# Performance work log

Hardware: AMD Instinct MI355X
Metric: run time of the kernel (lower is better)

## Reference

```python
import jax, jax.numpy as jnp
import numpy as np

H = 32          # hidden_size
L = 10          # linear_size
EPS = 1e-14


def _lstm_cell(x, h, c, Wih, Whh, bih, bhh):
    # torch LSTMCell: gates ordered [i, f, g, o]
    gates = x @ Wih.T + bih + h @ Whh.T + bhh
    i, f, g, o = jnp.split(gates, 4, axis=-1)
    i = jax.nn.sigmoid(i)
    f = jax.nn.sigmoid(f)
    g = jnp.tanh(g)
    o = jax.nn.sigmoid(o)
    c_new = f * c + i * g
    h_new = o * jnp.tanh(c_new)
    return h_new, c_new


def setup_inputs() -> dict:
    key = jax.random.key(0)
    ks = jax.random.split(key, 24)
    B, N = 8, 100000
    inp = {
        "x": jax.random.normal(ks[0], (B, N), jnp.float32),
        "grad": jax.random.normal(ks[1], (B, N), jnp.float32),
        "h0": jax.random.normal(ks[2], (B, N, H), jnp.float32),
        "c0": jax.random.normal(ks[3], (B, N, H), jnp.float32),
        "h1": jax.random.normal(ks[4], (B, N, H), jnp.float32),
        "c1": jax.random.normal(ks[5], (B, N, H), jnp.float32),
        # initial_transform: Linear(2, L) -> tanh -> Linear(L, L)
        "W1": jax.random.normal(ks[6], (L, 2), jnp.float32) * 0.3,
        "b1": jax.random.normal(ks[7], (L,), jnp.float32) * 0.1,
        "W2": jax.random.normal(ks[8], (L, L), jnp.float32) * 0.3,
        "b2": jax.random.normal(ks[9], (L,), jnp.float32) * 0.1,
        # LSTMCell layer 0 (input L) and layer 1 (input H)
        "Wih0": jax.random.normal(ks[10], (4 * H, L), jnp.float32) * 0.1,
        "Whh0": jax.random.normal(ks[11], (4 * H, H), jnp.float32) * 0.1,
        "bih0": jax.random.normal(ks[12], (4 * H,), jnp.float32) * 0.1,
        "bhh0": jax.random.normal(ks[13], (4 * H,), jnp.float32) * 0.1,
        "Wih1": jax.random.normal(ks[14], (4 * H, H), jnp.float32) * 0.1,
        "Whh1": jax.random.normal(ks[15], (4 * H, H), jnp.float32) * 0.1,
        "bih1": jax.random.normal(ks[16], (4 * H,), jnp.float32) * 0.1,
        "bhh1": jax.random.normal(ks[17], (4 * H,), jnp.float32) * 0.1,
        # fc: Linear(H, 1)
        "Wfc": jax.random.normal(ks[18], (1, H), jnp.float32) * 0.1,
        "bfc": jax.random.normal(ks[19], (1,), jnp.float32) * 0.1,
    }
    return inp


def reference(x, grad, h0, c0, h1, c1, W1, b1, W2, b2,
              Wih0, Whh0, bih0, bhh0, Wih1, Whh1, bih1, bhh1, Wfc, bfc):
    B, N = x.shape
    BN = B * N
    g = grad.reshape(BN, 1)
    # gradient preprocessing: [sign, log(|g| + eps)]
    inp = jnp.concatenate([jnp.sign(g), jnp.log(jnp.abs(g) + EPS)], axis=1)  # (BN, 2)
    t = jnp.tanh(inp @ W1.T + b1) @ W2.T + b2                                # (BN, L)
    # batched across all n variables simultaneously (no cross-variable recurrence)
    h0n, c0n = _lstm_cell(t, h0.reshape(BN, H), c0.reshape(BN, H), Wih0, Whh0, bih0, bhh0)
    h1n, c1n = _lstm_cell(h0n, h1.reshape(BN, H), c1.reshape(BN, H), Wih1, Whh1, bih1, bhh1)
    delta = (h1n @ Wfc.T + bfc).reshape(B, N)
    x_new = x + delta
    return (x_new,
            h0n.reshape(B, N, H), c0n.reshape(B, N, H),
            h1n.reshape(B, N, H), c1n.reshape(B, N, H),
            delta)
```

## Files before the change

### kernel.cpp

```cpp
#include <hip/hip_runtime.h>


typedef __attribute__((ext_vector_type(8))) short bf16x8;
typedef __attribute__((ext_vector_type(4))) float f32x4;

#define HH 32
#define LL 10
#define NG 128

__device__ __forceinline__ short f2bf(float x) {
  unsigned u = __float_as_uint(x);
  u += 0x7fffu + ((u >> 16) & 1u);
  return (short)(u >> 16);
}
__device__ __forceinline__ float fsig(float x) { return 1.0f / (1.0f + __expf(-x)); }
__device__ __forceinline__ float ftanh(float x) { return 2.0f / (1.0f + __expf(-2.0f * x)) - 1.0f; }

__global__ __launch_bounds__(256, 3) void l2o_fused(
    const float* __restrict__ x, const float* __restrict__ grad,
    const float* __restrict__ h0, const float* __restrict__ c0,
    const float* __restrict__ h1, const float* __restrict__ c1,
    const float* __restrict__ W1, const float* __restrict__ b1,
    const float* __restrict__ W2, const float* __restrict__ b2,
    const float* __restrict__ Wih0, const float* __restrict__ Whh0,
    const float* __restrict__ bih0, const float* __restrict__ bhh0,
    const float* __restrict__ Wih1, const float* __restrict__ Whh1,
    const float* __restrict__ bih1, const float* __restrict__ bhh1,
    const float* __restrict__ Wfc, const float* __restrict__ bfc,
    float* __restrict__ out, int BNi)
{
  const size_t BN = (size_t)BNi;
  float* __restrict__ xout  = out;
  float* __restrict__ h0out = out + BN;
  float* __restrict__ c0out = out + BN + BN * HH;
  float* __restrict__ h1out = out + BN + 2 * BN * HH;
  float* __restrict__ c1out = out + BN + 3 * BN * HH;
  float* __restrict__ dout  = out + BN + 4 * BN * HH;

  __shared__ __align__(16) short wih0L[2][NG][8];
  __shared__ __align__(16) short whh0L[4][NG][8];
  __shared__ __align__(16) short wih1L[4][NG][8];
  __shared__ __align__(16) short whh1L[4][NG][8];
  __shared__ __align__(16) short tsg[4][2][64][8];
  __shared__ __align__(16) short hsg[4][4][64][8];

  const int tid = threadIdx.x;
  for (int idx = tid; idx < NG * HH; idx += 256) {
    int n = idx >> 5, k = idx & 31;
    whh0L[k >> 3][n][k & 7] = f2bf(Whh0[n * HH + k]);
    wih1L[k >> 3][n][k & 7] = f2bf(Wih1[n * HH + k]);
    whh1L[k >> 3][n][k & 7] = f2bf(Whh1[n * HH + k]);
  }
  for (int idx = tid; idx < NG * 16; idx += 256) {
    int n = idx >> 4, k = idx & 15;
    wih0L[k >> 3][n][k & 7] = (k < LL) ? f2bf(Wih0[n * LL + k]) : (short)0;
  }

  const int lane = tid & 63;
  const int w = tid >> 6;
  const int col = lane & 15;
  const int g = lane >> 4;

  float biasv0[8], biasv1[8];
#pragma unroll
  for (int nt = 0; nt < 8; ++nt) {
    biasv0[nt] = bih0[nt * 16 + col] + bhh0[nt * 16 + col];
    biasv1[nt] = bih1[nt * 16 + col] + bhh1[nt * 16 + col];
  }
  const float wfc0 = Wfc[col], wfc1 = Wfc[16 + col];
  const float bfcv = bfc[0];

  const int ebase = blockIdx.x * 256 + w * 64;

  {
    float gv = grad[ebase + lane];
    float sg = (gv > 0.f) ? 1.f : ((gv < 0.f) ? -1.f : 0.f);
    float lg = __logf(fabsf(gv) + 1e-14f);
    float u[LL], t[LL];
#pragma unroll
    for (int j = 0; j < LL; ++j)
      u[j] = ftanh(W1[2 * j] * sg + W1[2 * j + 1] * lg + b1[j]);
#pragma unroll
    for (int j = 0; j < LL; ++j) {
      float a = b2[j];
#pragma unroll
      for (int k = 0; k < LL; ++k) a += W2[j * LL + k] * u[k];
      t[j] = a;
    }
    bf16x8 tv0, tv1;
#pragma unroll
    for (int s = 0; s < 8; ++s) tv0[s] = f2bf(t[s]);
    tv1[0] = f2bf(t[8]); tv1[1] = f2bf(t[9]);
#pragma unroll
    for (int s = 2; s < 8; ++s) tv1[s] = 0;
    *reinterpret_cast<bf16x8*>(&tsg[w][0][lane][0]) = tv0;
    *reinterpret_cast<bf16x8*>(&tsg[w][1][lane][0]) = tv1;
  }
  __syncthreads();

#pragma unroll 1
  for (int st = 0; st < 4; ++st) {
    const int m16 = ebase + st * 16;
    const int mrow = 4 * g;

    bf16x8 a_t = {0, 0, 0, 0, 0, 0, 0, 0};
    if (g < 2) a_t = *reinterpret_cast<const bf16x8*>(&tsg[w][g][st * 16 + col][0]);
    const float4* hp = reinterpret_cast<const float4*>(h0 + (size_t)(m16 + col) * HH + 8 * g);
    float4 v0 = hp[0], v1 = hp[1];
    bf16x8 a_h0;
    a_h0[0] = f2bf(v0.x); a_h0[1] = f2bf(v0.y); a_h0[2] = f2bf(v0.z); a_h0[3] = f2bf(v0.w);
    a_h0[4] = f2bf(v1.x); a_h0[5] = f2bf(v1.y); a_h0[6] = f2bf(v1.z); a_h0[7] = f2bf(v1.w);

    float c0r[2][4];
#pragma unroll
    for (int kk = 0; kk < 2; ++kk)
#pragma unroll
      for (int r = 0; r < 4; ++r)
        c0r[kk][r] = c0[(size_t)(m16 + mrow + r) * HH + kk * 16 + col];

    f32x4 acc[8];
#pragma unroll
    for (int nt = 0; nt < 8; ++nt) {
      float bv = biasv0[nt];
      f32x4 a = {bv, bv, bv, bv};
      acc[nt] = a;
    }
#pragma unroll
    for (int nt = 0; nt < 8; ++nt) {
      bf16x8 bih = {0, 0, 0, 0, 0, 0, 0, 0};
      if (g < 2) bih = *reinterpret_cast<const bf16x8*>(&wih0L[g][nt * 16 + col][0]);
      acc[nt] = __builtin_amdgcn_mfma_f32_16x16x32_bf16(a_t, bih, acc[nt], 0, 0, 0);
      bf16x8 bhh = *reinterpret_cast<const bf16x8*>(&whh0L[g][nt * 16 + col][0]);
      acc[nt] = __builtin_amdgcn_mfma_f32_16x16x32_bf16(a_h0, bhh, acc[nt], 0, 0, 0);
    }

#pragma unroll
    for (int kk = 0; kk < 2; ++kk) {
      const int k = kk * 16 + col;
#pragma unroll
      for (int r = 0; r < 4; ++r) {
        const size_t e2 = (size_t)(m16 + mrow + r);
        float iv = fsig(acc[0 + kk][r]);
        float fv = fsig(acc[2 + kk][r]);
        float gv = ftanh(acc[4 + kk][r]);
        float ov = fsig(acc[6 + kk][r]);
        float cn = fv * c0r[kk][r] + iv * gv;
        float hn = ov * ftanh(cn);
        c0out[e2 * HH + k] = cn;
        h0out[e2 * HH + k] = hn;
        hsg[w][k >> 3][st * 16 + mrow + r][k & 7] = f2bf(hn);
      }
    }
    __syncthreads();

    bf16x8 a_hn = *reinterpret_cast<const bf16x8*>(&hsg[w][g][st * 16 + col][0]);
    const float4* h1p = reinterpret_cast<const float4*>(h1 + (size_t)(m16 + col) * HH + 8 * g);
    float4 w0 = h1p[0], w1v = h1p[1];
    bf16x8 a_h1;
    a_h1[0] = f2bf(w0.x);  a_h1[1] = f2bf(w0.y);  a_h1[2] = f2bf(w0.z);  a_h1[3] = f2bf(w0.w);
    a_h1[4] = f2bf(w1v.x); a_h1[5] = f2bf(w1v.y); a_h1[6] = f2bf(w1v.z); a_h1[7] = f2bf(w1v.w);

    float c1r[2][4];
#pragma unroll
    for (int kk = 0; kk < 2; ++kk)
#pragma unroll
      for (int r = 0; r < 4; ++r)
        c1r[kk][r] = c1[(size_t)(m16 + mrow + r) * HH + kk * 16 + col];

#pragma unroll
    for (int nt = 0; nt < 8; ++nt) {
      float bv = biasv1[nt];
      f32x4 a = {bv, bv, bv, bv};
      acc[nt] = a;
    }
#pragma unroll
    for (int nt = 0; nt < 8; ++nt) {
      bf16x8 bih = *reinterpret_cast<const bf16x8*>(&wih1L[g][nt * 16 + col][0]);
      acc[nt] = __builtin_amdgcn_mfma_f32_16x16x32_bf16(a_hn, bih, acc[nt], 0, 0, 0);
      bf16x8 bhh = *reinterpret_cast<const bf16x8*>(&whh1L[g][nt * 16 + col][0]);
      acc[nt] = __builtin_amdgcn_mfma_f32_16x16x32_bf16(a_h1, bhh, acc[nt], 0, 0, 0);
    }

    float dsum[4] = {0.f, 0.f, 0.f, 0.f};
#pragma unroll
    for (int kk = 0; kk < 2; ++kk) {
      const int k = kk * 16 + col;
      const float wf = kk ? wfc1 : wfc0;
#pragma unroll
      for (int r = 0; r < 4; ++r) {
        const size_t e2 = (size_t)(m16 + mrow + r);
        float iv = fsig(acc[0 + kk][r]);
        float fv = fsig(acc[2 + kk][r]);
        float gv = ftanh(acc[4 + kk][r]);
        float ov = fsig(acc[6 + kk][r]);
        float cn = fv * c1r[kk][r] + iv * gv;
        float hn = ov * ftanh(cn);
        c1out[e2 * HH + k] = cn;
        h1out[e2 * HH + k] = hn;
        dsum[r] += hn * wf;
      }
    }
#pragma unroll
    for (int off = 1; off < 16; off <<= 1) {
#pragma unroll
      for (int r = 0; r < 4; ++r) dsum[r] += __shfl_xor(dsum[r], off, 64);
    }
    if (col == 0) {
      const int e4 = m16 + mrow;
      float4 xv = *reinterpret_cast<const float4*>(x + e4);
      float4 dv = {dsum[0] + bfcv, dsum[1] + bfcv, dsum[2] + bfcv, dsum[3] + bfcv};
      *reinterpret_cast<float4*>(dout + e4) = dv;
      float4 xn = {xv.x + dv.x, xv.y + dv.y, xv.z + dv.z, xv.w + dv.w};
      *reinterpret_cast<float4*>(xout + e4) = xn;
    }
  }
}

extern "C" void kernel_launch(void* const* d_in, const int* in_sizes, int n_in,
                              void* d_out, int out_size, void* d_ws, size_t ws_size,
                              hipStream_t stream) {
  const float* x    = (const float*)d_in[0];
  const float* grad = (const float*)d_in[1];
  const float* h0   = (const float*)d_in[2];
  const float* c0   = (const float*)d_in[3];
  const float* h1   = (const float*)d_in[4];
  const float* c1   = (const float*)d_in[5];
  const float* W1   = (const float*)d_in[6];
  const float* b1   = (const float*)d_in[7];
  const float* W2   = (const float*)d_in[8];
  const float* b2   = (const float*)d_in[9];
  const float* Wih0 = (const float*)d_in[10];
  const float* Whh0 = (const float*)d_in[11];
  const float* bih0 = (const float*)d_in[12];
  const float* bhh0 = (const float*)d_in[13];
  const float* Wih1 = (const float*)d_in[14];
  const float* Whh1 = (const float*)d_in[15];
  const float* bih1 = (const float*)d_in[16];
  const float* bhh1 = (const float*)d_in[17];
  const float* Wfc  = (const float*)d_in[18];
  const float* bfc  = (const float*)d_in[19];
  const int BN = in_sizes[0];
  const int nblk = BN / 256;
  l2o_fused<<<nblk, 256, 0, stream>>>(x, grad, h0, c0, h1, c1, W1, b1, W2, b2,
                                      Wih0, Whh0, bih0, bhh0, Wih1, Whh1,
                                      bih1, bhh1, Wfc, bfc, (float*)d_out, BN);
}
```

Baseline: 232.2 us.

## Hoist all global loads per step, drop block barrier, shrink LDS, raise occupancy

```diff
diff --git a/kernel.cpp b/kernel.cpp
--- a/kernel.cpp
+++ b/kernel.cpp
@@ -9,14 +9,17 @@
 #define NG 128
 
 __device__ __forceinline__ short f2bf(float x) {
-  unsigned u = __float_as_uint(x);
-  u += 0x7fffu + ((u >> 16) & 1u);
-  return (short)(u >> 16);
-}
-__device__ __forceinline__ float fsig(float x) { return 1.0f / (1.0f + __expf(-x)); }
-__device__ __forceinline__ float ftanh(float x) { return 2.0f / (1.0f + __expf(-2.0f * x)) - 1.0f; }
-
-__global__ __launch_bounds__(256, 3) void l2o_fused(
+  __bf16 b = (__bf16)x;
+  return __builtin_bit_cast(short, b);
+}
+__device__ __forceinline__ float fsig(float x) {
+  return __builtin_amdgcn_rcpf(1.0f + __expf(-x));
+}
+__device__ __forceinline__ float ftanh(float x) {
+  return fmaf(2.0f, __builtin_amdgcn_rcpf(1.0f + __expf(-2.0f * x)), -1.0f);
+}
+
+__global__ __launch_bounds__(256, 4) void l2o_fused(
     const float* __restrict__ x, const float* __restrict__ grad,
     const float* __restrict__ h0, const float* __restrict__ c0,
     const float* __restrict__ h1, const float* __restrict__ c1,
@@ -41,8 +44,9 @@
   __shared__ __align__(16) short whh0L[4][NG][8];
   __shared__ __align__(16) short wih1L[4][NG][8];
   __shared__ __align__(16) short whh1L[4][NG][8];
-  __shared__ __align__(16) short tsg[4][2][64][8];
-  __shared__ __align__(16) short hsg[4][4][64][8];
+  __shared__ __align__(16) short tsg0[4][64][8];
+  __shared__ __align__(4)  short tsg1[4][64][2];
+  __shared__ __align__(16) short hsg[4][4][16][8];
 
   const int tid = threadIdx.x;
   for (int idx = tid; idx < NG * HH; idx += 256) {
@@ -87,14 +91,12 @@
       for (int k = 0; k < LL; ++k) a += W2[j * LL + k] * u[k];
       t[j] = a;
     }
-    bf16x8 tv0, tv1;
+    bf16x8 tv0;
 #pragma unroll
     for (int s = 0; s < 8; ++s) tv0[s] = f2bf(t[s]);
-    tv1[0] = f2bf(t[8]); tv1[1] = f2bf(t[9]);
-#pragma unroll
-    for (int s = 2; s < 8; ++s) tv1[s] = 0;
-    *reinterpret_cast<bf16x8*>(&tsg[w][0][lane][0]) = tv0;
-    *reinterpret_cast<bf16x8*>(&tsg[w][1][lane][0]) = tv1;
+    *reinterpret_cast<bf16x8*>(&tsg0[w][lane][0]) = tv0;
+    tsg1[w][lane][0] = f2bf(t[8]);
+    tsg1[w][lane][1] = f2bf(t[9]);
   }
   __syncthreads();
 
@@ -103,20 +105,29 @@
     const int m16 = ebase + st * 16;
     const int mrow = 4 * g;
 
-    bf16x8 a_t = {0, 0, 0, 0, 0, 0, 0, 0};
-    if (g < 2) a_t = *reinterpret_cast<const bf16x8*>(&tsg[w][g][st * 16 + col][0]);
     const float4* hp = reinterpret_cast<const float4*>(h0 + (size_t)(m16 + col) * HH + 8 * g);
     float4 v0 = hp[0], v1 = hp[1];
+    const float4* h1p = reinterpret_cast<const float4*>(h1 + (size_t)(m16 + col) * HH + 8 * g);
+    float4 w0 = h1p[0], w1v = h1p[1];
+    float c0r[2][4], c1r[2][4];
+#pragma unroll
+    for (int kk = 0; kk < 2; ++kk)
+#pragma unroll
+      for (int r = 0; r < 4; ++r) {
+        c0r[kk][r] = c0[(size_t)(m16 + mrow + r) * HH + kk * 16 + col];
+        c1r[kk][r] = c1[(size_t)(m16 + mrow + r) * HH + kk * 16 + col];
+      }
+    float4 xv = *reinterpret_cast<const float4*>(x + m16 + mrow);
+
+    bf16x8 a_t = {0, 0, 0, 0, 0, 0, 0, 0};
+    if (g == 0) a_t = *reinterpret_cast<const bf16x8*>(&tsg0[w][st * 16 + col][0]);
+    else if (g == 1) {
+      a_t[0] = tsg1[w][st * 16 + col][0];
+      a_t[1] = tsg1[w][st * 16 + col][1];
+    }
     bf16x8 a_h0;
     a_h0[0] = f2bf(v0.x); a_h0[1] = f2bf(v0.y); a_h0[2] = f2bf(v0.z); a_h0[3] = f2bf(v0.w);
     a_h0[4] = f2bf(v1.x); a_h0[5] = f2bf(v1.y); a_h0[6] = f2bf(v1.z); a_h0[7] = f2bf(v1.w);
-
-    float c0r[2][4];
-#pragma unroll
-    for (int kk = 0; kk < 2; ++kk)
-#pragma unroll
-      for (int r = 0; r < 4; ++r)
-        c0r[kk][r] = c0[(size_t)(m16 + mrow + r) * HH + kk * 16 + col];
 
     f32x4 acc[8];
 #pragma unroll
@@ -148,24 +159,15 @@
         float hn = ov * ftanh(cn);
         c0out[e2 * HH + k] = cn;
         h0out[e2 * HH + k] = hn;
-        hsg[w][k >> 3][st * 16 + mrow + r][k & 7] = f2bf(hn);
+        hsg[w][k >> 3][mrow + r][k & 7] = f2bf(hn);
       }
     }
-    __syncthreads();
-
-    bf16x8 a_hn = *reinterpret_cast<const bf16x8*>(&hsg[w][g][st * 16 + col][0]);
-    const float4* h1p = reinterpret_cast<const float4*>(h1 + (size_t)(m16 + col) * HH + 8 * g);
-    float4 w0 = h1p[0], w1v = h1p[1];
+    asm volatile("s_waitcnt lgkmcnt(0)" ::: "memory");
+
+    bf16x8 a_hn = *reinterpret_cast<const bf16x8*>(&hsg[w][g][col][0]);
     bf16x8 a_h1;
     a_h1[0] = f2bf(w0.x);  a_h1[1] = f2bf(w0.y);  a_h1[2] = f2bf(w0.z);  a_h1[3] = f2bf(w0.w);
     a_h1[4] = f2bf(w1v.x); a_h1[5] = f2bf(w1v.y); a_h1[6] = f2bf(w1v.z); a_h1[7] = f2bf(w1v.w);
-
-    float c1r[2][4];
-#pragma unroll
-    for (int kk = 0; kk < 2; ++kk)
-#pragma unroll
-      for (int r = 0; r < 4; ++r)
-        c1r[kk][r] = c1[(size_t)(m16 + mrow + r) * HH + kk * 16 + col];
 
 #pragma unroll
     for (int nt = 0; nt < 8; ++nt) {
@@ -207,7 +209,6 @@
     }
     if (col == 0) {
       const int e4 = m16 + mrow;
-      float4 xv = *reinterpret_cast<const float4*>(x + e4);
       float4 dv = {dsum[0] + bfcv, dsum[1] + bfcv, dsum[2] + bfcv, dsum[3] + bfcv};
       *reinterpret_cast<float4*>(dout + e4) = dv;
       float4 xn = {xv.x + dv.x, xv.y + dv.y, xv.z + dv.z, xv.w + dv.w};
```

After: 290.0 us. 1.25x slower.
